# Optimization experiments

Hardware: AMD Instinct MI355X
Metric: run time of the kernel (lower is better)

Reference implementation:

```python
import jax, jax.numpy as jnp
import numpy as np
from jax import lax

DISCOUNT = 0.99
NORMALIZE = True
EPS = 1e-9


def setup_inputs() -> dict:
    key = jax.random.key(0)
    k1, k2 = jax.random.split(key)
    B, T = 4096, 8192
    rewards = jax.random.normal(k1, (B, T), dtype=jnp.float32)
    done_flags = (jax.random.uniform(k2, (B, T)) < 0.01).astype(jnp.float32)
    return {"rewards": rewards, "done_flags": done_flags}


def _episode_returns(rewards, done_flags):
    # reverse-time recurrence: r_t = rew_t + gamma * r_{t+1} * (1 - done_t)
    rw = jnp.moveaxis(rewards, -1, 0)      # [T, B]
    dn = jnp.moveaxis(done_flags, -1, 0)   # [T, B]

    def step(carry, xs):
        r, d = xs
        ret = r + DISCOUNT * carry * (1.0 - d)
        return ret, ret

    # init carry = 0 makes the last step reduce to returns[-1] = rewards[-1]
    _, rets = lax.scan(step, jnp.zeros_like(rw[0]), (rw, dn), reverse=True)
    returns = jnp.moveaxis(rets, 0, -1)    # [B, T]

    if NORMALIZE:
        # torch: (returns - returns.mean()) / (returns.std(dim=-1) + 1e-9)
        # global mean, per-trajectory std (unbiased, matching torch default)
        std = jnp.std(returns, axis=-1, ddof=1, keepdims=True)
        returns = (returns - jnp.mean(returns)) / (std + EPS)
    return returns


def reference(rewards, done_flags):
    return _episode_returns(rewards, done_flags)
```

## Files before the change

### kernel.cpp

```cpp
#include <hip/hip_runtime.h>
#include <math.h>

#define TLEN   8192
#define BROWS  4096
#define NT     256
#define WPB    (NT / 64)
#define GRID   (BROWS / WPB)
#define TPW    512
#define NTW    (TLEN / TPW)
#define GAMMA  0.99f
#define EPSN   1e-9

typedef float f4 __attribute__((ext_vector_type(4)));

__device__ __forceinline__ void scan_tile(const f4 r0, const f4 r1,
                                          const f4 d0, const f4 d1,
                                          const int lane, float& tc,
                                          float* __restrict__ dst,
                                          double& accS, double& accQ) {
  float rv[8], cv[8];
  rv[0] = r0.x; rv[1] = r0.y; rv[2] = r0.z; rv[3] = r0.w;
  rv[4] = r1.x; rv[5] = r1.y; rv[6] = r1.z; rv[7] = r1.w;
  cv[0] = fmaf(-GAMMA, d0.x, GAMMA);
  cv[1] = fmaf(-GAMMA, d0.y, GAMMA);
  cv[2] = fmaf(-GAMMA, d0.z, GAMMA);
  cv[3] = fmaf(-GAMMA, d0.w, GAMMA);
  cv[4] = fmaf(-GAMMA, d1.x, GAMMA);
  cv[5] = fmaf(-GAMMA, d1.y, GAMMA);
  cv[6] = fmaf(-GAMMA, d1.z, GAMMA);
  cv[7] = fmaf(-GAMMA, d1.w, GAMMA);

  float A = 0.f, P = 1.f;
#pragma unroll
  for (int j = 7; j >= 0; --j) {
    A = fmaf(cv[j], A, rv[j]);
    P *= cv[j];
    rv[j] = A;
    cv[j] = P;
  }

  float sA = A, sP = P;
#pragma unroll
  for (int d = 1; d < 64; d <<= 1) {
    const float tA = __shfl_down(sA, d);
    const float tP = __shfl_down(sP, d);
    if (lane + d < 64) { sA = fmaf(sP, tA, sA); sP *= tP; }
  }

  float eA = __shfl_down(sA, 1);
  float eP = __shfl_down(sP, 1);
  if (lane == 63) { eA = 0.f; eP = 1.f; }
  const float carry = fmaf(eP, tc, eA);

  const float gA = __shfl(sA, 0);
  const float gP = __shfl(sP, 0);
  tc = fmaf(gP, tc, gA);

  float fs = 0.f, fq = 0.f;
  float o[8];
#pragma unroll
  for (int j = 0; j < 8; ++j) {
    const float r = fmaf(cv[j], carry, rv[j]);
    o[j] = r;
    fs += r;
    fq  = fmaf(r, r, fq);
  }
  f4* go = (f4*)dst + 2 * lane;
  f4 o0; o0.x = o[0]; o0.y = o[1]; o0.z = o[2]; o0.w = o[3];
  f4 o1; o1.x = o[4]; o1.y = o[5]; o1.z = o[6]; o1.w = o[7];
  go[0] = o0;
  go[1] = o1;
  accS += (double)fs;
  accQ += (double)fq;
}

__global__ __launch_bounds__(NT, 4) void er_scan(const float* __restrict__ rew,
                                                 const float* __restrict__ don,
                                                 float* __restrict__ out,
                                                 double* __restrict__ rowSum,
                                                 float* __restrict__ rowInv) {
  const int tid  = threadIdx.x;
  const int lane = tid & 63;
  const int wv   = tid >> 6;
  const int row  = blockIdx.x * WPB + wv;
  const size_t rbase = (size_t)row * TLEN;

  const f4* gr = (const f4*)(rew + rbase);
  const f4* gd = (const f4*)(don + rbase);
  float* ob = out + rbase;

  f4 aR0, aR1, aD0, aD1, bR0, bR1, bD0, bD1;
  {
    const int f = (NTW - 1) * (TPW / 4) + 2 * lane;
    aR0 = gr[f]; aR1 = gr[f + 1];
    aD0 = gd[f]; aD1 = gd[f + 1];
  }

  float tc = 0.f;
  double accS = 0.0, accQ = 0.0;

#pragma unroll
  for (int kk = 0; kk < NTW / 2; ++kk) {
    const int k = NTW - 1 - 2 * kk;
    if (k >= 1) {
      const int f = (k - 1) * (TPW / 4) + 2 * lane;
      bR0 = gr[f]; bR1 = gr[f + 1];
      bD0 = gd[f]; bD1 = gd[f + 1];
    }
    __builtin_amdgcn_sched_barrier(0);
    scan_tile(aR0, aR1, aD0, aD1, lane, tc, ob + (size_t)k * TPW, accS, accQ);

    if (k >= 2) {
      const int f = (k - 2) * (TPW / 4) + 2 * lane;
      aR0 = gr[f]; aR1 = gr[f + 1];
      aD0 = gd[f]; aD1 = gd[f + 1];
    }
    __builtin_amdgcn_sched_barrier(0);
    scan_tile(bR0, bR1, bD0, bD1, lane, tc, ob + (size_t)(k - 1) * TPW, accS, accQ);
  }

  double ds = accS, dq = accQ;
#pragma unroll
  for (int d = 32; d >= 1; d >>= 1) {
    ds += __shfl_down(ds, d);
    dq += __shfl_down(dq, d);
  }
  if (lane == 0) {
    rowSum[row] = ds;
    double var = (dq - ds * ds / (double)TLEN) / (double)(TLEN - 1);
    if (var < 0.0) var = 0.0;
    rowInv[row] = (float)(1.0 / (sqrt(var) + EPSN));
  }
}

__global__ __launch_bounds__(256) void er_mean(const double* __restrict__ rowSum,
                                               float* __restrict__ meanPtr) {
  const int tid = threadIdx.x;
  double s = 0.0;
  for (int i = tid; i < BROWS; i += 256) s += rowSum[i];
#pragma unroll
  for (int d = 32; d >= 1; d >>= 1) s += __shfl_down(s, d);
  __shared__ double red[4];
  const int lane = tid & 63, wv = tid >> 6;
  if (lane == 0) red[wv] = s;
  __syncthreads();
  if (tid == 0) {
    const double t = red[0] + red[1] + red[2] + red[3];
    *meanPtr = (float)(t / ((double)BROWS * (double)TLEN));
  }
}

__global__ __launch_bounds__(256) void er_norm(float* __restrict__ out,
                                               const float* __restrict__ rowInv,
                                               const float* __restrict__ meanPtr) {
  const int row = blockIdx.x;
  const float mean = *meanPtr;
  const float inv  = rowInv[row];
  f4* o4 = (f4*)(out + (size_t)row * TLEN);
#pragma unroll
  for (int i = threadIdx.x; i < TLEN / 4; i += 256) {
    f4 v = o4[i];
    v.x = (v.x - mean) * inv;
    v.y = (v.y - mean) * inv;
    v.z = (v.z - mean) * inv;
    v.w = (v.w - mean) * inv;
    o4[i] = v;
  }
}

extern "C" void kernel_launch(void* const* d_in, const int* in_sizes, int n_in,
                              void* d_out, int out_size, void* d_ws, size_t ws_size,
                              hipStream_t stream) {
  const float* rew = (const float*)d_in[0];
  const float* don = (const float*)d_in[1];
  float* out = (float*)d_out;

  double* rowSum  = (double*)d_ws;
  float*  rowInv  = (float*)((char*)d_ws + BROWS * 8);
  float*  meanPtr = (float*)((char*)d_ws + BROWS * 8 + BROWS * 4);

  er_scan<<<GRID, NT, 0, stream>>>(rew, don, out, rowSum, rowInv);
  er_mean<<<1, 256, 0, stream>>>(rowSum, meanPtr);
  er_norm<<<BROWS, 256, 0, stream>>>(out, rowInv, meanPtr);
}
```

Baseline: 354.7 us.

## Shrink scan tile to 4 elements per lane with 4-deep load ring

The per-lane tile drops from 8 to 4 elements, so each wave handles 256-element tiles with one f4 load and store per lane. Prefetch moves from double buffering to a four-buffer ring that keeps loads two tiles ahead of compute. The goal is better coalescing of contiguous 1KB accesses and more loads in flight to hide memory latency. In exchange the number of wave-wide shuffle scans doubles, 32 tiles instead of 16, which adds cross-lane shuffle cost per element.

```diff
diff --git a/kernel.cpp b/kernel.cpp
--- a/kernel.cpp
+++ b/kernel.cpp
@@ -6,33 +6,27 @@
 #define NT     256
 #define WPB    (NT / 64)
 #define GRID   (BROWS / WPB)
-#define TPW    512
+#define TPW    256
 #define NTW    (TLEN / TPW)
 #define GAMMA  0.99f
 #define EPSN   1e-9
 
 typedef float f4 __attribute__((ext_vector_type(4)));
 
-__device__ __forceinline__ void scan_tile(const f4 r0, const f4 r1,
-                                          const f4 d0, const f4 d1,
-                                          const int lane, float& tc,
-                                          float* __restrict__ dst,
-                                          double& accS, double& accQ) {
-  float rv[8], cv[8];
-  rv[0] = r0.x; rv[1] = r0.y; rv[2] = r0.z; rv[3] = r0.w;
-  rv[4] = r1.x; rv[5] = r1.y; rv[6] = r1.z; rv[7] = r1.w;
-  cv[0] = fmaf(-GAMMA, d0.x, GAMMA);
-  cv[1] = fmaf(-GAMMA, d0.y, GAMMA);
-  cv[2] = fmaf(-GAMMA, d0.z, GAMMA);
-  cv[3] = fmaf(-GAMMA, d0.w, GAMMA);
-  cv[4] = fmaf(-GAMMA, d1.x, GAMMA);
-  cv[5] = fmaf(-GAMMA, d1.y, GAMMA);
-  cv[6] = fmaf(-GAMMA, d1.z, GAMMA);
-  cv[7] = fmaf(-GAMMA, d1.w, GAMMA);
+__device__ __forceinline__ void scan_tile4(const f4 r, const f4 d,
+                                           const int lane, float& tc,
+                                           float* __restrict__ dst,
+                                           double& accS, double& accQ) {
+  float rv[4], cv[4];
+  rv[0] = r.x; rv[1] = r.y; rv[2] = r.z; rv[3] = r.w;
+  cv[0] = fmaf(-GAMMA, d.x, GAMMA);
+  cv[1] = fmaf(-GAMMA, d.y, GAMMA);
+  cv[2] = fmaf(-GAMMA, d.z, GAMMA);
+  cv[3] = fmaf(-GAMMA, d.w, GAMMA);
 
   float A = 0.f, P = 1.f;
 #pragma unroll
-  for (int j = 7; j >= 0; --j) {
+  for (int j = 3; j >= 0; --j) {
     A = fmaf(cv[j], A, rv[j]);
     P *= cv[j];
     rv[j] = A;
@@ -41,10 +35,10 @@
 
   float sA = A, sP = P;
 #pragma unroll
-  for (int d = 1; d < 64; d <<= 1) {
-    const float tA = __shfl_down(sA, d);
-    const float tP = __shfl_down(sP, d);
-    if (lane + d < 64) { sA = fmaf(sP, tA, sA); sP *= tP; }
+  for (int dd = 1; dd < 64; dd <<= 1) {
+    const float tA = __shfl_down(sA, dd);
+    const float tP = __shfl_down(sP, dd);
+    if (lane + dd < 64) { sA = fmaf(sP, tA, sA); sP *= tP; }
   }
 
   float eA = __shfl_down(sA, 1);
@@ -57,19 +51,17 @@
   tc = fmaf(gP, tc, gA);
 
   float fs = 0.f, fq = 0.f;
-  float o[8];
-#pragma unroll
-  for (int j = 0; j < 8; ++j) {
-    const float r = fmaf(cv[j], carry, rv[j]);
-    o[j] = r;
-    fs += r;
-    fq  = fmaf(r, r, fq);
+  f4 o;
+  {
+    const float r0 = fmaf(cv[0], carry, rv[0]);
+    const float r1 = fmaf(cv[1], carry, rv[1]);
+    const float r2 = fmaf(cv[2], carry, rv[2]);
+    const float r3 = fmaf(cv[3], carry, rv[3]);
+    o.x = r0; o.y = r1; o.z = r2; o.w = r3;
+    fs = (r0 + r1) + (r2 + r3);
+    fq = fmaf(r0, r0, fmaf(r1, r1, fmaf(r2, r2, r3 * r3)));
   }
-  f4* go = (f4*)dst + 2 * lane;
-  f4 o0; o0.x = o[0]; o0.y = o[1]; o0.z = o[2]; o0.w = o[3];
-  f4 o1; o1.x = o[4]; o1.y = o[5]; o1.z = o[6]; o1.w = o[7];
-  go[0] = o0;
-  go[1] = o1;
+  ((f4*)dst)[lane] = o;
   accS += (double)fs;
   accQ += (double)fq;
 }
@@ -89,34 +81,31 @@
   const f4* gd = (const f4*)(don + rbase);
   float* ob = out + rbase;
 
-  f4 aR0, aR1, aD0, aD1, bR0, bR1, bD0, bD1;
-  {
-    const int f = (NTW - 1) * (TPW / 4) + 2 * lane;
-    aR0 = gr[f]; aR1 = gr[f + 1];
-    aD0 = gd[f]; aD1 = gd[f + 1];
-  }
+  f4 bR0, bR1, bR2, bR3, bD0, bD1, bD2, bD3;
 
-  float tc = 0.f;
+  bR3 = gr[31 * 64 + lane]; bD3 = gd[31 * 64 + lane];
+  bR2 = gr[30 * 64 + lane]; bD2 = gd[30 * 64 + lane];
+
   double accS = 0.0, accQ = 0.0;
+  float  tc = 0.f;
 
 #pragma unroll
-  for (int kk = 0; kk < NTW / 2; ++kk) {
-    const int k = NTW - 1 - 2 * kk;
-    if (k >= 1) {
-      const int f = (k - 1) * (TPW / 4) + 2 * lane;
-      bR0 = gr[f]; bR1 = gr[f + 1];
-      bD0 = gd[f]; bD1 = gd[f + 1];
-    }
+  for (int kb = 31; kb >= 3; kb -= 4) {
+    if (kb - 2 >= 0) { bR1 = gr[(kb - 2) * 64 + lane]; bD1 = gd[(kb - 2) * 64 + lane]; }
     __builtin_amdgcn_sched_barrier(0);
-    scan_tile(aR0, aR1, aD0, aD1, lane, tc, ob + (size_t)k * TPW, accS, accQ);
+    scan_tile4(bR3, bD3, lane, tc, ob + (size_t)kb * TPW, accS, accQ);
 
-    if (k >= 2) {
-      const int f = (k - 2) * (TPW / 4) + 2 * lane;
-      aR0 = gr[f]; aR1 = gr[f + 1];
-      aD0 = gd[f]; aD1 = gd[f + 1];
-    }
+    if (kb - 3 >= 0) { bR0 = gr[(kb - 3) * 64 + lane]; bD0 = gd[(kb - 3) * 64 + lane]; }
     __builtin_amdgcn_sched_barrier(0);
-    scan_tile(bR0, bR1, bD0, bD1, lane, tc, ob + (size_t)(k - 1) * TPW, accS, accQ);
+    scan_tile4(bR2, bD2, lane, tc, ob + (size_t)(kb - 1) * TPW, accS, accQ);
+
+    if (kb - 4 >= 0) { bR3 = gr[(kb - 4) * 64 + lane]; bD3 = gd[(kb - 4) * 64 + lane]; }
+    __builtin_amdgcn_sched_barrier(0);
+    scan_tile4(bR1, bD1, lane, tc, ob + (size_t)(kb - 2) * TPW, accS, accQ);
+
+    if (kb - 5 >= 0) { bR2 = gr[(kb - 5) * 64 + lane]; bD2 = gd[(kb - 5) * 64 + lane]; }
+    __builtin_amdgcn_sched_barrier(0);
+    scan_tile4(bR0, bD0, lane, tc, ob + (size_t)(kb - 3) * TPW, accS, accQ);
   }
 
   double ds = accS, dq = accQ;
```

Result: no change. 352.1 us (-0.7%).
